# Kernel optimization log

Hardware: AMD Instinct MI355X
Metric: run time of the kernel (lower is better)

Reference implementation:

```python
import jax, jax.numpy as jnp
import numpy as np

NUM_NODES = 50000
NUM_EDGES = 800000
HIDDEN = 128
HEADS = 8
HEAD_DIM = HIDDEN // HEADS  # 16
FF_HIDDEN = 4 * HIDDEN
LN_EPS = 1e-5


def _xavier(key, shape, gain=0.01):
    fan_out, fan_in = shape
    bound = gain * np.sqrt(6.0 / (fan_in + fan_out))
    return jax.random.uniform(key, shape, jnp.float32, -bound, bound)


def setup_inputs() -> dict:
    key = jax.random.key(0)
    ks = jax.random.split(key, 10)
    x = jax.random.normal(ks[0], (NUM_NODES, HIDDEN), jnp.float32)
    edge_index = jax.random.randint(ks[1], (2, NUM_EDGES), 0, NUM_NODES, jnp.int64)
    return {
        "x": x,
        "edge_index": edge_index,
        "Wq": _xavier(ks[2], (HIDDEN, HIDDEN)),
        "bq": jnp.zeros((HIDDEN,), jnp.float32),
        "Wk": _xavier(ks[3], (HIDDEN, HIDDEN)),
        "bk": jnp.zeros((HIDDEN,), jnp.float32),
        "Wv": _xavier(ks[4], (HIDDEN, HIDDEN)),
        "bv": jnp.zeros((HIDDEN,), jnp.float32),
        "Wo": _xavier(ks[5], (HIDDEN, HIDDEN)),
        "bo": jnp.zeros((HIDDEN,), jnp.float32),
        "W1": _xavier(ks[6], (FF_HIDDEN, HIDDEN)),
        "b1": jnp.zeros((FF_HIDDEN,), jnp.float32),
        "W2": _xavier(ks[7], (HIDDEN, FF_HIDDEN)),
        "b2": jnp.zeros((HIDDEN,), jnp.float32),
        "g1": jnp.ones((HIDDEN,), jnp.float32),
        "be1": jnp.zeros((HIDDEN,), jnp.float32),
        "g2": jnp.ones((HIDDEN,), jnp.float32),
        "be2": jnp.zeros((HIDDEN,), jnp.float32),
    }


def _layernorm(v, g, b):
    mu = jnp.mean(v, axis=-1, keepdims=True)
    var = jnp.mean(jnp.square(v - mu), axis=-1, keepdims=True)
    return (v - mu) * jax.lax.rsqrt(var + LN_EPS) * g + b


def _forward(x, edge_index, Wq, bq, Wk, bk, Wv, bv, Wo, bo, W1, b1, W2, b2, g1, be1, g2, be2):
    src = edge_index[0]  # key/value side (_j)
    dst = edge_index[1]  # query side (_i), aggregation index
    scale = 1.0 / np.sqrt(HEAD_DIM)

    # Euclidean manifold: GeometricLinear == plain linear
    q = (x @ Wq.T + bq).reshape(NUM_NODES, HEADS, HEAD_DIM)
    k = (x @ Wk.T + bk).reshape(NUM_NODES, HEADS, HEAD_DIM)
    v = (x @ Wv.T + bv).reshape(NUM_NODES, HEADS, HEAD_DIM)

    # per-edge attention scores [E, H]
    alpha = jnp.einsum('ehd,ehd->eh', q[dst], k[src]) * scale
    # segment softmax over destination nodes
    m = jax.ops.segment_max(alpha, dst, num_segments=NUM_NODES)  # [N, H]
    ea = jnp.exp(alpha - m[dst])
    denom = jax.ops.segment_sum(ea, dst, num_segments=NUM_NODES)  # [N, H]
    alpha = ea / (denom[dst] + 1e-16)

    # scatter-add weighted values -> [N, H, D]
    agg = jax.ops.segment_sum(v[src] * alpha[..., None], dst, num_segments=NUM_NODES)
    att = agg.reshape(NUM_NODES, HIDDEN) @ Wo.T + bo

    # residual + norm1 (Euclidean)
    h = _layernorm(x + att, g1, be1)

    # feed-forward: fc1 -> exact GELU -> fc2
    ff = (jax.nn.gelu(h @ W1.T + b1, approximate=False)) @ W2.T + b2

    # residual + norm2
    return _layernorm(h + ff, g2, be2)


def reference(x, edge_index, Wq, bq, Wk, bk, Wv, bv, Wo, bo, W1, b1, W2, b2, g1, be1, g2, be2):
    return _forward(x, edge_index, Wq, bq, Wk, bk, Wv, bv, Wo, bo, W1, b1, W2, b2, g1, be1, g2, be2)
```

## Files before the change

### kernel.cpp

```cpp
#include <hip/hip_runtime.h>
#include <math.h>

#define N_HEADS 8
#define HEAD_DIM 16
#define HID 128
#define QKV_ROWB 512

typedef unsigned short ushort_t;
typedef __attribute__((ext_vector_type(8))) short short8;
typedef __attribute__((ext_vector_type(4))) float floatx4;
typedef __attribute__((ext_vector_type(2))) float f32x2;

#define KV_SCALE 64.0f
#define KV_INV_SCALE 0.015625f

#define W2_SCALE 65536.0f
#define A1_SCALE 512.0f
#define FF2_DESCALE (1.0f / 33554432.0f)

__device__ __forceinline__ ushort_t f2bf(float f) {
    unsigned u = __float_as_uint(f);
    unsigned r = (u + 0x7FFFu + ((u >> 16) & 1u)) >> 16;
    return (ushort_t)r;
}
__device__ __forceinline__ float bf2f(ushort_t u) {
    return __uint_as_float(((unsigned)u) << 16);
}

__device__ __forceinline__ void gld_lds16(const void* g, void* l) {
    __builtin_amdgcn_global_load_lds(
        (const __attribute__((address_space(1))) void*)g,
        (__attribute__((address_space(3))) void*)l, 16, 0, 0);
}

__device__ __forceinline__ float gelu_f(float x) {
    float z = fabsf(x) * 0.70710678118654752f;
    float t = 1.0f / (1.0f + 0.3275911f * z);
    float y = t * (0.254829592f + t * (-0.284496736f + t * (1.421413741f
            + t * (-1.453152027f + t * 1.061405429f))));
    float e = 1.0f - y * __expf(-z * z);
    e = copysignf(e, x);
    return 0.5f * x * (1.0f + e);
}

__global__ __launch_bounds__(256)
void prep_kernel(const float* __restrict__ x,
                 const float* __restrict__ Wq, const float* __restrict__ Wk,
                 const float* __restrict__ Wv, const float* __restrict__ Wo,
                 const float* __restrict__ W1, const float* __restrict__ W2,
                 const float* __restrict__ bq, const float* __restrict__ bk,
                 const float* __restrict__ bv,
                 const int* __restrict__ dst, int* __restrict__ cnt, int E,
                 ushort_t* __restrict__ xb, ushort_t* __restrict__ wts,
                 float* __restrict__ bqkv,
                 ushort_t* __restrict__ w1frag,
                 unsigned char* __restrict__ w2frag8, int xpairs)
{
    int i = blockIdx.x * 256 + threadIdx.x;
    if (i < xpairs) {
        float2 v = ((const float2*)x)[i];
        xb[i * 2]     = f2bf(v.x);
        xb[i * 2 + 1] = f2bf(v.y);
        return;
    }
    int j = i - xpairs;
    if (j < 32768) {
        const float* s; int off;
        if (j < 8192)       { s = Wq; off = j; }
        else if (j < 16384) { s = Wk; off = j - 8192; }
        else if (j < 24576) { s = Wv; off = j - 16384; }
        else                { s = Wo; off = j - 24576; }
        float2 v = ((const float2*)s)[off];
        wts[j * 2]     = f2bf(v.x);
        wts[j * 2 + 1] = f2bf(v.y);
        return;
    }
    int b = j - 32768;
    if (b < 384) {
        bqkv[b] = (b < 128) ? bq[b] : (b < 256) ? bk[b - 128] : bv[b - 256];
        return;
    }
    int c = b - 384;
    if (c < 8192) {
        int lane = c & 63, tk = c >> 6;
        int t16 = tk >> 2, kst = tk & 3;
        int row = t16 * 16 + (lane & 15);
        int kb  = kst * 32 + (lane >> 4) * 8;
        const float* s = W1 + (size_t)row * HID + kb;
        ushort_t* d = w1frag + (size_t)c * 8;
#pragma unroll
        for (int e = 0; e < 8; ++e) d[e] = f2bf(s[e]);
        return;
    }
    int c2 = c - 8192;
    if (c2 < 8192) {
        int lane = c2 & 63, tk = c2 >> 6;
        int t16 = tk >> 4, kst = tk & 15;
        int row = t16 * 16 + (lane & 15);
        int kb  = kst * 32 + (lane >> 4) * 8;
        const float* s = W2 + (size_t)row * 512 + kb;
        unsigned u0 = 0, u1 = 0;
        u0 = __builtin_amdgcn_cvt_pk_fp8_f32(s[0]*W2_SCALE, s[1]*W2_SCALE, u0, false);
        u0 = __builtin_amdgcn_cvt_pk_fp8_f32(s[2]*W2_SCALE, s[3]*W2_SCALE, u0, true);
        u1 = __builtin_amdgcn_cvt_pk_fp8_f32(s[4]*W2_SCALE, s[5]*W2_SCALE, u1, false);
        u1 = __builtin_amdgcn_cvt_pk_fp8_f32(s[6]*W2_SCALE, s[7]*W2_SCALE, u1, true);
        uint2 o; o.x = u0; o.y = u1;
        *(uint2*)(w2frag8 + (size_t)c2 * 8) = o;
        return;
    }
    int e = c2 - 8192;
    if (e < E) atomicAdd(&cnt[dst[e]], 1);
}

template<int MT, int ACT, int LN, int OUTF>
__global__ __launch_bounds__(256)
void gemm_t(const ushort_t* __restrict__ A, int lda, int M,
            const ushort_t* __restrict__ W, int K,
            const float* __restrict__ bias,
            ushort_t* __restrict__ hfragp, ushort_t* __restrict__ outb, int ostride,
            const float* __restrict__ resf, const ushort_t* __restrict__ resb,
            const float* __restrict__ g, const float* __restrict__ be)
{
    constexpr int MI   = MT / 32;
    constexpr int HALF = MT * 64 + 128 * 64;
    constexpr int BNC  = MT * 136;
    constexpr int SB   = (2 * HALF > BNC) ? 2 * HALF : BNC;
    __shared__ __align__(16) ushort_t sbuf[SB];
    __shared__ float pS[LN ? MT : 1][2];
    __shared__ float pQ[LN ? MT : 1][2];

    const int tid  = threadIdx.x;
    const int wave = tid >> 6, lane = tid & 63;
    const int gm0 = blockIdx.x * MT;
    const int o0  = blockIdx.y * 128;
    const int mhalf = wave >> 1, ohalf = wave & 1;

    auto stage = [&](int kc, int h) {
        ushort_t* As = sbuf + h * HALF;
        ushort_t* Ws = As + MT * 64;
#pragma unroll
        for (int it = 0; it < 4; ++it) {
            int s   = it * 256 + tid;
            int ln  = s & 63;
            int grp = s >> 6;
            int tile = grp >> 1, kst = grp & 1;
            int row = tile * 16 + (ln & 15);
            int kk  = kst * 32 + (ln >> 4) * 8;
            gld_lds16(&W[(size_t)(o0 + row) * K + kc + kk],
                      &Ws[(it * 256 + wave * 64) * 8]);
        }
#pragma unroll
        for (int it = 0; it < MT / 32; ++it) {
            int s   = it * 256 + tid;
            int ln  = s & 63;
            int grp = s >> 6;
            int tile = grp >> 1, kst = grp & 1;
            int row = tile * 16 + (ln & 15);
            int kk  = kst * 32 + (ln >> 4) * 8;
            int ar = gm0 + row; if (ar >= M) ar = M - 1;
            gld_lds16(&A[(size_t)ar * lda + kc + kk],
                      &As[(it * 256 + wave * 64) * 8]);
        }
    };

    floatx4 acc[MI][4];
#pragma unroll
    for (int i = 0; i < MI; ++i)
#pragma unroll
        for (int j = 0; j < 4; ++j) acc[i][j] = (floatx4)(0.f);

    const int nk = K >> 6;
    stage(0, 0);
    __syncthreads();
    for (int t = 0; t < nk; ++t) {
        if (t + 1 < nk) stage((t + 1) * 64, (t + 1) & 1);
        const ushort_t* As = sbuf + (t & 1) * HALF;
        const ushort_t* Ws = As + MT * 64;
#pragma unroll
        for (int kst = 0; kst < 2; ++kst) {
            short8 af[MI], wf[4];
#pragma unroll
            for (int i = 0; i < MI; ++i) {
                int mt = mhalf * MI + i;
                af[i] = *(const short8*)&As[((mt * 2 + kst) * 64 + lane) * 8];
            }
#pragma unroll
            for (int j = 0; j < 4; ++j) {
                int ot = ohalf * 4 + j;
                wf[j] = *(const short8*)&Ws[((ot * 2 + kst) * 64 + lane) * 8];
            }
#pragma unroll
            for (int i = 0; i < MI; ++i)
#pragma unroll
                for (int j = 0; j < 4; ++j)
                    acc[i][j] = __builtin_amdgcn_mfma_f32_16x16x32_bf16(
                        af[i], wf[j], acc[i][j], 0, 0, 0);
        }
        __syncthreads();
    }

    ushort_t* B16 = sbuf;

    if (LN) {
#pragma unroll
        for (int j = 0; j < 4; ++j) {
            int oc = (ohalf * 4 + j) * 16 + (lane & 15);
            float bj = bias[oc];
#pragma unroll
            for (int i = 0; i < MI; ++i) {
                int rbase = gm0 + (mhalf * MI + i) * 16 + (lane >> 4) * 4;
#pragma unroll
                for (int r = 0; r < 4; ++r) {
                    int rowc = rbase + r; if (rowc >= M) rowc = M - 1;
                    float rv = resb ? bf2f(resb[(size_t)rowc * HID + oc])
                                    : resf[(size_t)rowc * HID + oc];
                    acc[i][j][r] += bj + rv;
                }
            }
        }
#pragma unroll
        for (int i = 0; i < MI; ++i) {
#pragma unroll
            for (int r = 0; r < 4; ++r) {
                float s1 = acc[i][0][r] + acc[i][1][r] + acc[i][2][r] + acc[i][3][r];
                float s2 = acc[i][0][r] * acc[i][0][r] + acc[i][1][r] * acc[i][1][r]
                         + acc[i][2][r] * acc[i][2][r] + acc[i][3][r] * acc[i][3][r];
                s1 += __shfl_xor(s1, 1); s1 += __shfl_xor(s1, 2);
                s1 += __shfl_xor(s1, 4); s1 += __shfl_xor(s1, 8);
                s2 += __shfl_xor(s2, 1); s2 += __shfl_xor(s2, 2);
                s2 += __shfl_xor(s2, 4); s2 += __shfl_xor(s2, 8);
                if ((lane & 15) == 0) {
                    int rl = (mhalf * MI + i) * 16 + (lane >> 4) * 4 + r;
                    pS[rl][ohalf] = s1;
                    pQ[rl][ohalf] = s2;
                }
            }
        }
        __syncthreads();
#pragma unroll
        for (int i = 0; i < MI; ++i) {
#pragma unroll
            for (int r = 0; r < 4; ++r) {
                int rl = (mhalf * MI + i) * 16 + (lane >> 4) * 4 + r;
                float S = pS[rl][0] + pS[rl][1];
                float Q = pQ[rl][0] + pQ[rl][1];
                float mu = S * (1.f / 128.f);
                float var = Q * (1.f / 128.f) - mu * mu;
                float rstd = rsqrtf(var + 1e-5f);
#pragma unroll
                for (int j = 0; j < 4; ++j) {
                    int oc = (ohalf * 4 + j) * 16 + (lane & 15);
                    acc[i][j][r] = (acc[i][j][r] - mu) * rstd * g[oc] + be[oc];
                }
            }
        }
        __syncthreads();
    }

    if (OUTF == 0 || (OUTF == 3 && blockIdx.y == 0)) {
#pragma unroll
        for (int i = 0; i < MI; ++i)
#pragma unroll
            for (int j = 0; j < 4; ++j) {
                int oc = (ohalf * 4 + j) * 16 + (lane & 15);
                float bj = LN ? 0.f : bias[o0 + oc];
#pragma unroll
                for (int r = 0; r < 4; ++r) {
                    int rl = (mhalf * MI + i) * 16 + (lane >> 4) * 4 + r;
                    float v = acc[i][j][r] + bj;
                    if (ACT) v = gelu_f(v);
                    B16[rl * 136 + oc] = f2bf(v);
                }
            }
        __syncthreads();
        const int oo = (OUTF == 3) ? 0 : o0;
#pragma unroll
        for (int p = 0; p < MT / 16; ++p) {
            int row = p * 16 + (tid >> 4);
            int ch  = tid & 15;
            if (gm0 + row < M)
                *(short8*)&outb[(size_t)(gm0 + row) * ostride + oo + ch * 8] =
                    *(const short8*)&B16[row * 136 + ch * 8];
        }
        if (LN && hfragp) {
            int kst = tid >> 6, ln = tid & 63;
#pragma unroll
            for (int p = 0; p < MT / 16; ++p) {
                if (gm0 + p * 16 < M) {
                    int gt = (gm0 >> 4) + p;
                    short8 v = *(const short8*)&B16[(p * 16 + (ln & 15)) * 136
                                                    + kst * 32 + (ln >> 4) * 8];
                    *(short8*)&hfragp[(((size_t)gt * 4 + kst) * 64 + ln) * 8] = v;
                }
            }
        }
    } else if (OUTF == 3) {
#pragma unroll
        for (int i = 0; i < MI; ++i)
#pragma unroll
            for (int j = 0; j < 4; ++j) {
                int oc = (ohalf * 4 + j) * 16 + (lane & 15);
                float bj = bias[o0 + oc];
#pragma unroll
                for (int r = 0; r < 4; ++r) {
                    int rl = (mhalf * MI + i) * 16 + (lane >> 4) * 4 + r;
                    float v = (acc[i][j][r] + bj) * KV_SCALE;
                    B16[rl * 136 + oc] = f2bf(v);
                }
            }
        __syncthreads();
        const int koff = (blockIdx.y - 1) * 8;
#pragma unroll
        for (int p = 0; p < MT / 16; ++p) {
            int row = p * 16 + (tid >> 4);
            int ch  = tid & 15;
            if (gm0 + row < M) {
                short8 s = *(const short8*)&B16[row * 136 + ch * 8];
                unsigned u0 = 0, u1 = 0;
                u0 = __builtin_amdgcn_cvt_pk_fp8_f32(
                         bf2f((ushort_t)s[0]), bf2f((ushort_t)s[1]), u0, false);
                u0 = __builtin_amdgcn_cvt_pk_fp8_f32(
                         bf2f((ushort_t)s[2]), bf2f((ushort_t)s[3]), u0, true);
                u1 = __builtin_amdgcn_cvt_pk_fp8_f32(
                         bf2f((ushort_t)s[4]), bf2f((ushort_t)s[5]), u1, false);
                u1 = __builtin_amdgcn_cvt_pk_fp8_f32(
                         bf2f((ushort_t)s[6]), bf2f((ushort_t)s[7]), u1, true);
                uint2 o; o.x = u0; o.y = u1;
                *(uint2*)((char*)outb + (size_t)(gm0 + row) * QKV_ROWB
                          + 256 + ch * 16 + koff) = o;
            }
        }
    }
}

__global__ __launch_bounds__(256)
void ff1w_kernel(const ushort_t* __restrict__ hfrag,
                 const ushort_t* __restrict__ w1frag,
                 const float* __restrict__ b1,
                 unsigned char* __restrict__ a1img, int M)
{
    __shared__ __align__(16) ushort_t sT[4][16 * 136];
    const int wave = threadIdx.x >> 6, lane = threadIdx.x & 63;
    const int cg = wave;
    const int nt16 = (M + 15) / 16;
    const int gt0 = blockIdx.x * 2;
    const int gt1 = gt0 + 1;
    const int gt1c = (gt1 < nt16) ? gt1 : nt16 - 1;
    const int l15 = lane & 15, l4 = lane >> 4;

    floatx4 acc[2][8];
#pragma unroll
    for (int i = 0; i < 2; ++i)
#pragma unroll
        for (int j = 0; j < 8; ++j) acc[i][j] = (floatx4)(0.f);

#pragma unroll
    for (int kst = 0; kst < 4; ++kst) {
        short8 a0 = *(const short8*)&hfrag[(((size_t)gt0  * 4 + kst) * 64 + lane) * 8];
        short8 a1 = *(const short8*)&hfrag[(((size_t)gt1c * 4 + kst) * 64 + lane) * 8];
        short8 bv[8];
#pragma unroll
        for (int j = 0; j < 8; ++j)
            bv[j] = *(const short8*)&w1frag[((((size_t)cg * 8 + j) * 4 + kst) * 64 + lane) * 8];
#pragma unroll
        for (int j = 0; j < 8; ++j) {
            acc[0][j] = __builtin_amdgcn_mfma_f32_16x16x32_bf16(a0, bv[j], acc[0][j], 0, 0, 0);
            acc[1][j] = __builtin_amdgcn_mfma_f32_16x16x32_bf16(a1, bv[j], acc[1][j], 0, 0, 0);
        }
    }

    float b1v[8];
#pragma unroll
    for (int j = 0; j < 8; ++j) b1v[j] = b1[cg * 128 + j * 16 + l15];

#pragma unroll
    for (int i = 0; i < 2; ++i) {
        const int gt = i ? gt1 : gt0;
#pragma unroll
        for (int j = 0; j < 8; ++j)
#pragma unroll
            for (int r = 0; r < 4; ++r)
                sT[wave][(l4 * 4 + r) * 136 + j * 16 + l15] =
                    f2bf(gelu_f(acc[i][j][r] + b1v[j]));
        if (gt < nt16) {
#pragma unroll
            for (int q = 0; q < 4; ++q) {
                float v[8];
#pragma unroll
                for (int e = 0; e < 8; ++e)
                    v[e] = bf2f(sT[wave][l15 * 136 + q * 32 + l4 * 8 + e]) * A1_SCALE;
                unsigned u0 = 0, u1 = 0;
                u0 = __builtin_amdgcn_cvt_pk_fp8_f32(v[0], v[1], u0, false);
                u0 = __builtin_amdgcn_cvt_pk_fp8_f32(v[2], v[3], u0, true);
                u1 = __builtin_amdgcn_cvt_pk_fp8_f32(v[4], v[5], u1, false);
                u1 = __builtin_amdgcn_cvt_pk_fp8_f32(v[6], v[7], u1, true);
                uint2 o; o.x = u0; o.y = u1;
                *(uint2*)(a1img + (((size_t)gt * 16 + cg * 4 + q) * 64 + lane) * 8) = o;
            }
        }
    }
}

__global__ __launch_bounds__(256)
void ff2w_kernel(const unsigned char* __restrict__ a1img,
                 const unsigned char* __restrict__ w2frag8,
                 const ushort_t* __restrict__ hb,
                 const float* __restrict__ b2,
                 const float* __restrict__ g, const float* __restrict__ be,
                 float* __restrict__ out, int M)
{
    const int wave = threadIdx.x >> 6, lane = threadIdx.x & 63;
    const int t32 = blockIdx.x * 4 + wave;
    const int nt32 = (M + 31) / 32;
    if (t32 >= nt32) return;
    const int nt16 = (M + 15) / 16;
    const int gt0 = t32 * 2;
    const int gt1c = (gt0 + 1 < nt16) ? gt0 + 1 : nt16 - 1;
    const int l15 = lane & 15, l4 = lane >> 4;

    floatx4 acc[2][8];
#pragma unroll
    for (int i = 0; i < 2; ++i)
#pragma unroll
        for (int j = 0; j < 8; ++j) acc[i][j] = (floatx4)(0.f);

#pragma unroll
    for (int kst = 0; kst < 16; ++kst) {
        long a0 = *(const long*)(a1img + (((size_t)gt0  * 16 + kst) * 64 + lane) * 8);
        long a1 = *(const long*)(a1img + (((size_t)gt1c * 16 + kst) * 64 + lane) * 8);
        long bv[8];
#pragma unroll
        for (int j = 0; j < 8; ++j)
            bv[j] = *(const long*)(w2frag8 + (((size_t)j * 16 + kst) * 64 + lane) * 8);
#pragma unroll
        for (int j = 0; j < 8; ++j) {
            acc[0][j] = __builtin_amdgcn_mfma_f32_16x16x32_fp8_fp8(a0, bv[j], acc[0][j], 0, 0, 0);
            acc[1][j] = __builtin_amdgcn_mfma_f32_16x16x32_fp8_fp8(a1, bv[j], acc[1][j], 0, 0, 0);
        }
    }

    float b2v[8], gv[8], bev[8];
#pragma unroll
    for (int j = 0; j < 8; ++j) {
        int oc = j * 16 + l15;
        b2v[j] = b2[oc]; gv[j] = g[oc]; bev[j] = be[oc];
    }

#pragma unroll
    for (int i = 0; i < 2; ++i) {
        const int rb = (t32 * 2 + i) * 16;
#pragma unroll
        for (int j = 0; j < 8; ++j) {
            int oc = j * 16 + l15;
#pragma unroll
            for (int r = 0; r < 4; ++r) {
                int row = rb + l4 * 4 + r;
                int rc = (row < M) ? row : M - 1;
                acc[i][j][r] = acc[i][j][r] * FF2_DESCALE + b2v[j]
                             + bf2f(hb[(size_t)rc * HID + oc]);
            }
        }
#pragma unroll
        for (int r = 0; r < 4; ++r) {
            float s1 = 0.f, s2 = 0.f;
#pragma unroll
            for (int j = 0; j < 8; ++j) {
                s1 += acc[i][j][r];
                s2 += acc[i][j][r] * acc[i][j][r];
            }
            s1 += __shfl_xor(s1, 1); s1 += __shfl_xor(s1, 2);
            s1 += __shfl_xor(s1, 4); s1 += __shfl_xor(s1, 8);
            s2 += __shfl_xor(s2, 1); s2 += __shfl_xor(s2, 2);
            s2 += __shfl_xor(s2, 4); s2 += __shfl_xor(s2, 8);
            float mu = s1 * (1.f / 128.f);
            float var = s2 * (1.f / 128.f) - mu * mu;
            float rstd = rsqrtf(var + 1e-5f);
            int row = rb + l4 * 4 + r;
            if (row < M) {
#pragma unroll
                for (int j = 0; j < 8; ++j)
                    out[(size_t)row * HID + j * 16 + l15] =
                        (acc[i][j][r] - mu) * rstd * gv[j] + bev[j];
            }
        }
    }
}

__global__ __launch_bounds__(256)
void scan1_kernel(const int* __restrict__ cnt, int* __restrict__ parts, int N)
{
    __shared__ int sd[256];
    int t = threadIdx.x;
    int base = blockIdx.x * 1024 + t * 4;
    int s = 0;
#pragma unroll
    for (int j = 0; j < 4; ++j) if (base + j < N) s += cnt[base + j];
    sd[t] = s; __syncthreads();
    for (int off = 128; off; off >>= 1) {
        if (t < off) sd[t] += sd[t + off];
        __syncthreads();
    }
    if (t == 0) parts[blockIdx.x] = sd[0];
}

__global__ __launch_bounds__(256)
void scan2_kernel(const int* __restrict__ parts, int* __restrict__ poff, int nb)
{
    __shared__ int sd[256];
    int t = threadIdx.x;
    int v = (t < nb) ? parts[t] : 0;
    sd[t] = v; __syncthreads();
    for (int off = 1; off < 256; off <<= 1) {
        int u = (t >= off) ? sd[t - off] : 0;
        __syncthreads();
        sd[t] += u;
        __syncthreads();
    }
    if (t < nb) poff[t] = sd[t] - v;
}

__global__ __launch_bounds__(256)
void scan3_kernel(const int* __restrict__ cnt, const int* __restrict__ poff,
                  int* __restrict__ rp, int N)
{
    __shared__ int sd[256];
    int t = threadIdx.x;
    int base = blockIdx.x * 1024 + t * 4;
    int v0 = (base + 0 < N) ? cnt[base + 0] : 0;
    int v1 = (base + 1 < N) ? cnt[base + 1] : 0;
    int v2 = (base + 2 < N) ? cnt[base + 2] : 0;
    int v3 = (base + 3 < N) ? cnt[base + 3] : 0;
    int s = v0 + v1 + v2 + v3;
    sd[t] = s; __syncthreads();
    for (int off = 1; off < 256; off <<= 1) {
        int u = (t >= off) ? sd[t - off] : 0;
        __syncthreads();
        sd[t] += u;
        __syncthreads();
    }
    int o = poff[blockIdx.x] + sd[t] - s;
    if (base + 0 < N) rp[base + 0] = o;
    if (base + 1 < N) rp[base + 1] = o + v0;
    if (base + 2 < N) rp[base + 2] = o + v0 + v1;
    if (base + 3 < N) rp[base + 3] = o + v0 + v1 + v2;
}

__global__ __launch_bounds__(256)
void scatter_kernel(const int* __restrict__ src, const int* __restrict__ dst,
                    int* __restrict__ rp, int* __restrict__ ssrc, int E, int N)
{
    int coh = blockIdx.x & 7;
    int bc  = blockIdx.x >> 3;
    int rr  = (N + 7) >> 3;
    int nlo = coh * rr;
    int nhi = nlo + rr; if (nhi > N) nhi = N;
    int stride = (gridDim.x >> 3) * 256;
    for (int e = bc * 256 + threadIdx.x; e < E; e += stride) {
        int d = dst[e];
        if (d >= nlo && d < nhi) {
            int pos = atomicAdd(&rp[d], 1);
            ssrc[pos] = src[e];
        }
    }
}

__global__ __launch_bounds__(256)
void attn_fused_kernel(const ushort_t* __restrict__ qkvb, const int* __restrict__ rp,
                       const int* __restrict__ ssrc, ushort_t* __restrict__ aggb, int N)
{
    int wave = threadIdx.x >> 6, lane = threadIdx.x & 63;
    int n = blockIdx.x * 4 + wave;
    if (n >= N) return;
    int grp = lane >> 4;
    int cb  = (lane & 15) * 16;
    const char* base = (const char*)qkvb;

    short8 qv = *(const short8*)(base + n * QKV_ROWB + cb);
    float q[8];
#pragma unroll
    for (int j = 0; j < 8; ++j) q[j] = bf2f((ushort_t)qv[j]) * (0.25f / KV_SCALE);

    int r0 = n ? rp[n - 1] : 0;
    int r1 = rp[n];
    float acc[8] = {0.f, 0.f, 0.f, 0.f, 0.f, 0.f, 0.f, 0.f};
    float l = 0.f;

    int r = r0;
    for (; r + 8 <= r1; r += 8) {
        int s0 = ssrc[r + grp];
        int s1 = ssrc[r + 4 + grp];
        uint4 kv0 = *(const uint4*)(base + s0 * QKV_ROWB + 256 + cb);
        uint4 kv1 = *(const uint4*)(base + s1 * QKV_ROWB + 256 + cb);

        f32x2 a0 = __builtin_amdgcn_cvt_pk_f32_fp8(kv0.x, false);
        f32x2 a1 = __builtin_amdgcn_cvt_pk_f32_fp8(kv0.x, true);
        f32x2 a2 = __builtin_amdgcn_cvt_pk_f32_fp8(kv0.y, false);
        f32x2 a3 = __builtin_amdgcn_cvt_pk_f32_fp8(kv0.y, true);
        f32x2 b0 = __builtin_amdgcn_cvt_pk_f32_fp8(kv1.x, false);
        f32x2 b1 = __builtin_amdgcn_cvt_pk_f32_fp8(kv1.x, true);
        f32x2 b2 = __builtin_amdgcn_cvt_pk_f32_fp8(kv1.y, false);
        f32x2 b3 = __builtin_amdgcn_cvt_pk_f32_fp8(kv1.y, true);

        float p0 = 0.f, p1 = 0.f;
        p0 = fmaf(q[0], a0.x, p0); p0 = fmaf(q[1], a0.y, p0);
        p0 = fmaf(q[2], a1.x, p0); p0 = fmaf(q[3], a1.y, p0);
        p0 = fmaf(q[4], a2.x, p0); p0 = fmaf(q[5], a2.y, p0);
        p0 = fmaf(q[6], a3.x, p0); p0 = fmaf(q[7], a3.y, p0);
        p1 = fmaf(q[0], b0.x, p1); p1 = fmaf(q[1], b0.y, p1);
        p1 = fmaf(q[2], b1.x, p1); p1 = fmaf(q[3], b1.y, p1);
        p1 = fmaf(q[4], b2.x, p1); p1 = fmaf(q[5], b2.y, p1);
        p1 = fmaf(q[6], b3.x, p1); p1 = fmaf(q[7], b3.y, p1);

        p0 += __shfl_xor(p0, 1);
        p1 += __shfl_xor(p1, 1);
        float e0 = __expf(p0), e1 = __expf(p1);
        l += e0 + e1;

        f32x2 v0 = __builtin_amdgcn_cvt_pk_f32_fp8(kv0.z, false);
        f32x2 v1 = __builtin_amdgcn_cvt_pk_f32_fp8(kv0.z, true);
        f32x2 v2 = __builtin_amdgcn_cvt_pk_f32_fp8(kv0.w, false);
        f32x2 v3 = __builtin_amdgcn_cvt_pk_f32_fp8(kv0.w, true);
        f32x2 w0 = __builtin_amdgcn_cvt_pk_f32_fp8(kv1.z, false);
        f32x2 w1 = __builtin_amdgcn_cvt_pk_f32_fp8(kv1.z, true);
        f32x2 w2 = __builtin_amdgcn_cvt_pk_f32_fp8(kv1.w, false);
        f32x2 w3 = __builtin_amdgcn_cvt_pk_f32_fp8(kv1.w, true);

        acc[0] = fmaf(e0, v0.x, acc[0]); acc[1] = fmaf(e0, v0.y, acc[1]);
        acc[2] = fmaf(e0, v1.x, acc[2]); acc[3] = fmaf(e0, v1.y, acc[3]);
        acc[4] = fmaf(e0, v2.x, acc[4]); acc[5] = fmaf(e0, v2.y, acc[5]);
        acc[6] = fmaf(e0, v3.x, acc[6]); acc[7] = fmaf(e0, v3.y, acc[7]);
        acc[0] = fmaf(e1, w0.x, acc[0]); acc[1] = fmaf(e1, w0.y, acc[1]);
        acc[2] = fmaf(e1, w1.x, acc[2]); acc[3] = fmaf(e1, w1.y, acc[3]);
        acc[4] = fmaf(e1, w2.x, acc[4]); acc[5] = fmaf(e1, w2.y, acc[5]);
        acc[6] = fmaf(e1, w3.x, acc[6]); acc[7] = fmaf(e1, w3.y, acc[7]);
    }
    for (; r < r1; r += 4) {
        int e = r + grp;
        int s = ssrc[(e < r1) ? e : r0];
        uint4 kv = *(const uint4*)(base + s * QKV_ROWB + 256 + cb);
        f32x2 a0 = __builtin_amdgcn_cvt_pk_f32_fp8(kv.x, false);
        f32x2 a1 = __builtin_amdgcn_cvt_pk_f32_fp8(kv.x, true);
        f32x2 a2 = __builtin_amdgcn_cvt_pk_f32_fp8(kv.y, false);
        f32x2 a3 = __builtin_amdgcn_cvt_pk_f32_fp8(kv.y, true);
        float p = 0.f;
        p = fmaf(q[0], a0.x, p); p = fmaf(q[1], a0.y, p);
        p = fmaf(q[2], a1.x, p); p = fmaf(q[3], a1.y, p);
        p = fmaf(q[4], a2.x, p); p = fmaf(q[5], a2.y, p);
        p = fmaf(q[6], a3.x, p); p = fmaf(q[7], a3.y, p);
        p += __shfl_xor(p, 1);
        float ea = (e < r1) ? __expf(p) : 0.f;
        l += ea;
        f32x2 v0 = __builtin_amdgcn_cvt_pk_f32_fp8(kv.z, false);
        f32x2 v1 = __builtin_amdgcn_cvt_pk_f32_fp8(kv.z, true);
        f32x2 v2 = __builtin_amdgcn_cvt_pk_f32_fp8(kv.w, false);
        f32x2 v3 = __builtin_amdgcn_cvt_pk_f32_fp8(kv.w, true);
        acc[0] = fmaf(ea, v0.x, acc[0]); acc[1] = fmaf(ea, v0.y, acc[1]);
        acc[2] = fmaf(ea, v1.x, acc[2]); acc[3] = fmaf(ea, v1.y, acc[3]);
        acc[4] = fmaf(ea, v2.x, acc[4]); acc[5] = fmaf(ea, v2.y, acc[5]);
        acc[6] = fmaf(ea, v3.x, acc[6]); acc[7] = fmaf(ea, v3.y, acc[7]);
    }

#pragma unroll
    for (int j = 0; j < 8; ++j) {
        acc[j] += __shfl_xor(acc[j], 16);
        acc[j] += __shfl_xor(acc[j], 32);
    }
    l += __shfl_xor(l, 16);
    l += __shfl_xor(l, 32);
    float inv = KV_INV_SCALE / (l + 1e-16f);
    if (grp == 0) {
        short8 o;
#pragma unroll
        for (int j = 0; j < 8; ++j) o[j] = (short)f2bf(acc[j] * inv);
        *(short8*)((char*)aggb + n * 256 + cb) = o;
    }
}

extern "C" void kernel_launch(void* const* d_in, const int* in_sizes, int n_in,
                              void* d_out, int out_size, void* d_ws, size_t ws_size,
                              hipStream_t stream)
{
    const float* x  = (const float*)d_in[0];
    const int*   ei = (const int*)d_in[1];
    const float* Wq = (const float*)d_in[2];
    const float* bq = (const float*)d_in[3];
    const float* Wk = (const float*)d_in[4];
    const float* bk = (const float*)d_in[5];
    const float* Wv = (const float*)d_in[6];
    const float* bv = (const float*)d_in[7];
    const float* Wo = (const float*)d_in[8];
    const float* bo = (const float*)d_in[9];
    const float* W1 = (const float*)d_in[10];
    const float* b1 = (const float*)d_in[11];
    const float* W2 = (const float*)d_in[12];
    const float* b2 = (const float*)d_in[13];
    const float* g1 = (const float*)d_in[14];
    const float* be1= (const float*)d_in[15];
    const float* g2 = (const float*)d_in[16];
    const float* be2= (const float*)d_in[17];
    float* out = (float*)d_out;

    const int N = in_sizes[0] / HID;
    const int E = in_sizes[1] / 2;
    const int* srcp = ei;
    const int* dstp = ei + E;

    const size_t NH = (size_t)N * HID;
    float* wsf = (float*)d_ws;

    ushort_t* xb    = (ushort_t*)wsf;
    ushort_t* qkvb  = (ushort_t*)(wsf + NH / 2);
    ushort_t* hfrag = (ushort_t*)(wsf + NH + NH / 2);
    ushort_t* aggb  = (ushort_t*)(wsf + 2 * NH);
    ushort_t* hb    = (ushort_t*)wsf;
    unsigned char* a1img = (unsigned char*)(wsf + NH / 2);

    ushort_t* wts    = (ushort_t*)(wsf + 2 * NH + NH / 2);
    ushort_t* w1frag = wts + 65536;
    unsigned char* w2frag8 = (unsigned char*)(w1frag + 65536);
    float*    bqkv = (float*)(w2frag8 + 65536);
    int*      rp   = (int*)(bqkv + 384);
    int*      cnt  = rp + (N + 1);
    int*      poff = cnt + N;
    int*      parts= poff + 256;
    int*      ssrc = parts + 256;

    hipMemsetAsync(cnt, 0, N * sizeof(int), stream);
    const int xpairs = (int)(NH / 2);
    const int ptot   = xpairs + 32768 + 384 + 8192 + 8192 + E;
    prep_kernel<<<(ptot + 255) / 256, 256, 0, stream>>>(
        x, Wq, Wk, Wv, Wo, W1, W2, bq, bk, bv, dstp, cnt, E,
        xb, wts, bqkv, w1frag, w2frag8, xpairs);

    const int nb = (N + 1023) / 1024;
    scan1_kernel<<<nb, 256, 0, stream>>>(cnt, parts, N);
    scan2_kernel<<<1, 256, 0, stream>>>(parts, poff, nb);
    scan3_kernel<<<nb, 256, 0, stream>>>(cnt, poff, rp, N);
    scatter_kernel<<<2048, 256, 0, stream>>>(srcp, dstp, rp, ssrc, E, N);

    const int gx64 = (N + 63) / 64;
    const int nt32 = (N + 31) / 32;

    gemm_t<64, 0, 0, 3><<<dim3(gx64, 3), 256, 0, stream>>>(
        xb, HID, N, wts, HID, bqkv, nullptr, qkvb, 256,
        nullptr, nullptr, nullptr, nullptr);

    attn_fused_kernel<<<(N + 3) / 4, 256, 0, stream>>>(qkvb, rp, ssrc, aggb, N);

    gemm_t<64, 0, 1, 0><<<dim3(gx64, 1), 256, 0, stream>>>(
        aggb, HID, N, wts + 49152, HID, bo, hfrag, hb, HID,
        x, nullptr, g1, be1);

    ff1w_kernel<<<nt32, 256, 0, stream>>>(hfrag, w1frag, b1, a1img, N);

    ff2w_kernel<<<(nt32 + 3) / 4, 256, 0, stream>>>(
        a1img, w2frag8, hb, b2, g2, be2, out, N);
}
```

Before: 323.9 us.

## Replace QKV GEMM with fragment-layout wave kernel and split edge counting

Converts x and Wq/Wk/Wv into MFMA-fragment-ordered bf16 layouts in the prep kernel. A new qkvw_kernel then loads operands directly into registers without an LDS staging loop, and each wave computes two 16-row tiles against all 128 output columns. Destination-degree counting moves out of prep into a separate count_kernel whose blocks each handle only atomics landing in one eighth of the node range. The goal is to improve atomic locality and cut the generic GEMM's shared-memory traffic. The cost is re-reading dst eight times and an extra launch.

```diff
diff --git a/kernel.cpp b/kernel.cpp
--- a/kernel.cpp
+++ b/kernel.cpp
@@ -50,46 +50,61 @@
                  const float* __restrict__ W1, const float* __restrict__ W2,
                  const float* __restrict__ bq, const float* __restrict__ bk,
                  const float* __restrict__ bv,
-                 const int* __restrict__ dst, int* __restrict__ cnt, int E,
-                 ushort_t* __restrict__ xb, ushort_t* __restrict__ wts,
-                 float* __restrict__ bqkv,
+                 ushort_t* __restrict__ xfrag, ushort_t* __restrict__ woB,
+                 ushort_t* __restrict__ wqkvf,
                  ushort_t* __restrict__ w1frag,
-                 unsigned char* __restrict__ w2frag8, int xpairs)
+                 unsigned char* __restrict__ w2frag8,
+                 float* __restrict__ bqkv, int xchunks)
 {
     int i = blockIdx.x * 256 + threadIdx.x;
-    if (i < xpairs) {
-        float2 v = ((const float2*)x)[i];
-        xb[i * 2]     = f2bf(v.x);
-        xb[i * 2 + 1] = f2bf(v.y);
+    if (i < xchunks) {
+        int t16 = i >> 8;
+        int rem = i & 255;
+        int lane = rem & 63;
+        int row = t16 * 16 + (lane & 15);
+        int k   = (rem >> 6) * 32 + (lane >> 4) * 8;
+        const float* s = x + (size_t)row * HID + k;
+        short8 v;
+#pragma unroll
+        for (int e = 0; e < 8; ++e) v[e] = (short)f2bf(s[e]);
+        *(short8*)(xfrag + (size_t)i * 8) = v;
         return;
     }
-    int j = i - xpairs;
-    if (j < 32768) {
-        const float* s; int off;
-        if (j < 8192)       { s = Wq; off = j; }
-        else if (j < 16384) { s = Wk; off = j - 8192; }
-        else if (j < 24576) { s = Wv; off = j - 16384; }
-        else                { s = Wo; off = j - 24576; }
-        float2 v = ((const float2*)s)[off];
-        wts[j * 2]     = f2bf(v.x);
-        wts[j * 2 + 1] = f2bf(v.y);
+    int j = i - xchunks;
+    if (j < 8192) {
+        float2 v = ((const float2*)Wo)[j];
+        woB[j * 2]     = f2bf(v.x);
+        woB[j * 2 + 1] = f2bf(v.y);
         return;
     }
-    int b = j - 32768;
-    if (b < 384) {
-        bqkv[b] = (b < 128) ? bq[b] : (b < 256) ? bk[b - 128] : bv[b - 256];
+    int b = j - 8192;
+    if (b < 6144) {
+        int w = b >> 11;
+        int rem = b & 2047;
+        int t16 = rem >> 8;
+        int rem2 = rem & 255;
+        int lane = rem2 & 63;
+        int row = t16 * 16 + (lane & 15);
+        int k   = ((rem2 >> 6) & 3) * 32 + (lane >> 4) * 8;
+        const float* W = (w == 0) ? Wq : (w == 1) ? Wk : Wv;
+        const float* s = W + (size_t)row * HID + k;
+        short8 v;
+#pragma unroll
+        for (int e = 0; e < 8; ++e) v[e] = (short)f2bf(s[e]);
+        *(short8*)(wqkvf + (size_t)b * 8) = v;
         return;
     }
-    int c = b - 384;
+    int c = b - 6144;
     if (c < 8192) {
         int lane = c & 63, tk = c >> 6;
         int t16 = tk >> 2, kst = tk & 3;
         int row = t16 * 16 + (lane & 15);
         int kb  = kst * 32 + (lane >> 4) * 8;
         const float* s = W1 + (size_t)row * HID + kb;
-        ushort_t* d = w1frag + (size_t)c * 8;
-#pragma unroll
-        for (int e = 0; e < 8; ++e) d[e] = f2bf(s[e]);
+        short8 v;
+#pragma unroll
+        for (int e = 0; e < 8; ++e) v[e] = (short)f2bf(s[e]);
+        *(short8*)(w1frag + (size_t)c * 8) = v;
         return;
     }
     int c2 = c - 8192;
@@ -108,8 +123,108 @@
         *(uint2*)(w2frag8 + (size_t)c2 * 8) = o;
         return;
     }
-    int e = c2 - 8192;
-    if (e < E) atomicAdd(&cnt[dst[e]], 1);
+    int d = c2 - 8192;
+    if (d < 384) {
+        bqkv[d] = (d < 128) ? bq[d] : (d < 256) ? bk[d - 128] : bv[d - 256];
+    }
+}
+
+__global__ __launch_bounds__(256)
+void count_kernel(const int* __restrict__ dst, int* __restrict__ cnt, int E, int N)
+{
+    int coh = blockIdx.x & 7;
+    int bc  = blockIdx.x >> 3;
+    int rr  = (N + 7) >> 3;
+    int nlo = coh * rr;
+    int nhi = nlo + rr; if (nhi > N) nhi = N;
+    int stride = (gridDim.x >> 3) * 256;
+    for (int e = bc * 256 + threadIdx.x; e < E; e += stride) {
+        int d = dst[e];
+        if (d >= nlo && d < nhi) atomicAdd(&cnt[d], 1);
+    }
+}
+
+__global__ __launch_bounds__(256)
+void qkvw_kernel(const ushort_t* __restrict__ xfrag,
+                 const ushort_t* __restrict__ wqkvf,
+                 const float* __restrict__ bqkv,
+                 ushort_t* __restrict__ qkvb, int nt16)
+{
+    __shared__ __align__(16) ushort_t sT[4][16 * 136];
+    const int wave = threadIdx.x >> 6, lane = threadIdx.x & 63;
+    const int y = blockIdx.y;
+    const int l15 = lane & 15, l4 = lane >> 4;
+    const int gt0 = blockIdx.x * 8 + wave * 2;
+    const int gt0c = (gt0 < nt16) ? gt0 : nt16 - 1;
+    const int gt1c = (gt0 + 1 < nt16) ? gt0 + 1 : nt16 - 1;
+
+    floatx4 acc[2][8];
+#pragma unroll
+    for (int i = 0; i < 2; ++i)
+#pragma unroll
+        for (int j = 0; j < 8; ++j) acc[i][j] = (floatx4)(0.f);
+
+    const ushort_t* wf = wqkvf + (size_t)y * 16384;
+#pragma unroll
+    for (int kst = 0; kst < 4; ++kst) {
+        short8 a0 = *(const short8*)&xfrag[(((size_t)gt0c * 4 + kst) * 64 + lane) * 8];
+        short8 a1 = *(const short8*)&xfrag[(((size_t)gt1c * 4 + kst) * 64 + lane) * 8];
+        short8 bv[8];
+#pragma unroll
+        for (int j = 0; j < 8; ++j)
+            bv[j] = *(const short8*)&wf[(((size_t)j * 4 + kst) * 64 + lane) * 8];
+#pragma unroll
+        for (int j = 0; j < 8; ++j) {
+            acc[0][j] = __builtin_amdgcn_mfma_f32_16x16x32_bf16(a0, bv[j], acc[0][j], 0, 0, 0);
+            acc[1][j] = __builtin_amdgcn_mfma_f32_16x16x32_bf16(a1, bv[j], acc[1][j], 0, 0, 0);
+        }
+    }
+
+    float bb[8];
+#pragma unroll
+    for (int j = 0; j < 8; ++j) bb[j] = bqkv[y * 128 + j * 16 + l15];
+
+#pragma unroll
+    for (int i = 0; i < 2; ++i) {
+        const int gt = gt0 + i;
+#pragma unroll
+        for (int j = 0; j < 8; ++j)
+#pragma unroll
+            for (int r = 0; r < 4; ++r) {
+                float v = acc[i][j][r] + bb[j];
+                if (y) v *= KV_SCALE;
+                sT[wave][(l4 * 4 + r) * 136 + j * 16 + l15] = f2bf(v);
+            }
+        if (gt < nt16) {
+            if (y == 0) {
+#pragma unroll
+                for (int c = 0; c < 4; ++c) {
+                    int ch = l4 * 4 + c;
+                    *(short8*)&qkvb[(size_t)(gt * 16 + l15) * 256 + ch * 8] =
+                        *(const short8*)&sT[wave][l15 * 136 + ch * 8];
+                }
+            } else {
+                const int koff = (y - 1) * 8;
+#pragma unroll
+                for (int c = 0; c < 4; ++c) {
+                    int ch = l4 * 4 + c;
+                    short8 s = *(const short8*)&sT[wave][l15 * 136 + ch * 8];
+                    unsigned u0 = 0, u1 = 0;
+                    u0 = __builtin_amdgcn_cvt_pk_fp8_f32(
+                             bf2f((ushort_t)s[0]), bf2f((ushort_t)s[1]), u0, false);
+                    u0 = __builtin_amdgcn_cvt_pk_fp8_f32(
+                             bf2f((ushort_t)s[2]), bf2f((ushort_t)s[3]), u0, true);
+                    u1 = __builtin_amdgcn_cvt_pk_fp8_f32(
+                             bf2f((ushort_t)s[4]), bf2f((ushort_t)s[5]), u1, false);
+                    u1 = __builtin_amdgcn_cvt_pk_fp8_f32(
+                             bf2f((ushort_t)s[6]), bf2f((ushort_t)s[7]), u1, true);
+                    uint2 o; o.x = u0; o.y = u1;
+                    *(uint2*)((char*)qkvb + (size_t)(gt * 16 + l15) * QKV_ROWB
+                              + 256 + ch * 16 + koff) = o;
+                }
+            }
+        }
+    }
 }
 
 template<int MT, int ACT, int LN, int OUTF>
@@ -257,77 +372,38 @@
         __syncthreads();
     }
 
-    if (OUTF == 0 || (OUTF == 3 && blockIdx.y == 0)) {
-#pragma unroll
-        for (int i = 0; i < MI; ++i)
-#pragma unroll
-            for (int j = 0; j < 4; ++j) {
-                int oc = (ohalf * 4 + j) * 16 + (lane & 15);
-                float bj = LN ? 0.f : bias[o0 + oc];
-#pragma unroll
-                for (int r = 0; r < 4; ++r) {
-                    int rl = (mhalf * MI + i) * 16 + (lane >> 4) * 4 + r;
-                    float v = acc[i][j][r] + bj;
-                    if (ACT) v = gelu_f(v);
-                    B16[rl * 136 + oc] = f2bf(v);
-                }
-            }
-        __syncthreads();
-        const int oo = (OUTF == 3) ? 0 : o0;
+#pragma unroll
+    for (int i = 0; i < MI; ++i)
+#pragma unroll
+        for (int j = 0; j < 4; ++j) {
+            int oc = (ohalf * 4 + j) * 16 + (lane & 15);
+            float bj = LN ? 0.f : bias[o0 + oc];
+#pragma unroll
+            for (int r = 0; r < 4; ++r) {
+                int rl = (mhalf * MI + i) * 16 + (lane >> 4) * 4 + r;
+                float v = acc[i][j][r] + bj;
+                if (ACT) v = gelu_f(v);
+                B16[rl * 136 + oc] = f2bf(v);
+            }
+        }
+    __syncthreads();
+#pragma unroll
+    for (int p = 0; p < MT / 16; ++p) {
+        int row = p * 16 + (tid >> 4);
+        int ch  = tid & 15;
+        if (gm0 + row < M)
+            *(short8*)&outb[(size_t)(gm0 + row) * ostride + o0 + ch * 8] =
+                *(const short8*)&B16[row * 136 + ch * 8];
+    }
+    if (LN && hfragp) {
+        int kst = tid >> 6, ln = tid & 63;
 #pragma unroll
         for (int p = 0; p < MT / 16; ++p) {
-            int row = p * 16 + (tid >> 4);
-            int ch  = tid & 15;
-            if (gm0 + row < M)
-                *(short8*)&outb[(size_t)(gm0 + row) * ostride + oo + ch * 8] =
-                    *(const short8*)&B16[row * 136 + ch * 8];
-        }
-        if (LN && hfragp) {
-            int kst = tid >> 6, ln = tid & 63;
-#pragma unroll
-            for (int p = 0; p < MT / 16; ++p) {
-                if (gm0 + p * 16 < M) {
-                    int gt = (gm0 >> 4) + p;
-                    short8 v = *(const short8*)&B16[(p * 16 + (ln & 15)) * 136
-                                                    + kst * 32 + (ln >> 4) * 8];
-                    *(short8*)&hfragp[(((size_t)gt * 4 + kst) * 64 + ln) * 8] = v;
-                }
-            }
-        }
-    } else if (OUTF == 3) {
-#pragma unroll
-        for (int i = 0; i < MI; ++i)
-#pragma unroll
-            for (int j = 0; j < 4; ++j) {
-                int oc = (ohalf * 4 + j) * 16 + (lane & 15);
-                float bj = bias[o0 + oc];
-#pragma unroll
-                for (int r = 0; r < 4; ++r) {
-                    int rl = (mhalf * MI + i) * 16 + (lane >> 4) * 4 + r;
-                    float v = (acc[i][j][r] + bj) * KV_SCALE;
-                    B16[rl * 136 + oc] = f2bf(v);
-                }
-            }
-        __syncthreads();
-        const int koff = (blockIdx.y - 1) * 8;
-#pragma unroll
-        for (int p = 0; p < MT / 16; ++p) {
-            int row = p * 16 + (tid >> 4);
-            int ch  = tid & 15;
-            if (gm0 + row < M) {
-                short8 s = *(const short8*)&B16[row * 136 + ch * 8];
-                unsigned u0 = 0, u1 = 0;
-                u0 = __builtin_amdgcn_cvt_pk_fp8_f32(
-                         bf2f((ushort_t)s[0]), bf2f((ushort_t)s[1]), u0, false);
-                u0 = __builtin_amdgcn_cvt_pk_fp8_f32(
-                         bf2f((ushort_t)s[2]), bf2f((ushort_t)s[3]), u0, true);
-                u1 = __builtin_amdgcn_cvt_pk_fp8_f32(
-                         bf2f((ushort_t)s[4]), bf2f((ushort_t)s[5]), u1, false);
-                u1 = __builtin_amdgcn_cvt_pk_fp8_f32(
-                         bf2f((ushort_t)s[6]), bf2f((ushort_t)s[7]), u1, true);
-                uint2 o; o.x = u0; o.y = u1;
-                *(uint2*)((char*)outb + (size_t)(gm0 + row) * QKV_ROWB
-                          + 256 + ch * 16 + koff) = o;
+            if (gm0 + p * 16 < M) {
+                int gt = (gm0 >> 4) + p;
+                short8 v = *(const short8*)&B16[(p * 16 + (ln & 15)) * 136
+                                                + kst * 32 + (ln >> 4) * 8];
+                *(short8*)&hfragp[(((size_t)gt * 4 + kst) * 64 + ln) * 8] = v;
             }
         }
     }
@@ -708,16 +784,21 @@
     const size_t NH = (size_t)N * HID;
     float* wsf = (float*)d_ws;
 
-    ushort_t* xb    = (ushort_t*)wsf;
+    const int nt16 = (N + 15) / 16;
+    const int nt32 = (N + 31) / 32;
+
+    ushort_t* xfrag = (ushort_t*)wsf;
     ushort_t* qkvb  = (ushort_t*)(wsf + NH / 2);
     ushort_t* hfrag = (ushort_t*)(wsf + NH + NH / 2);
     ushort_t* aggb  = (ushort_t*)(wsf + 2 * NH);
     ushort_t* hb    = (ushort_t*)wsf;
     unsigned char* a1img = (unsigned char*)(wsf + NH / 2);
 
-    ushort_t* wts    = (ushort_t*)(wsf + 2 * NH + NH / 2);
-    ushort_t* w1frag = wts + 65536;
-    unsigned char* w2frag8 = (unsigned char*)(w1frag + 65536);
+    ushort_t* U       = (ushort_t*)(wsf + 2 * NH + NH / 2);
+    ushort_t* woB     = U;
+    ushort_t* wqkvf   = U + 16384;
+    ushort_t* w1frag  = U + 65536;
+    unsigned char* w2frag8 = (unsigned char*)(U + 131072);
     float*    bqkv = (float*)(w2frag8 + 65536);
     int*      rp   = (int*)(bqkv + 384);
     int*      cnt  = rp + (N + 1);
@@ -726,29 +807,27 @@
     int*      ssrc = parts + 256;
 
     hipMemsetAsync(cnt, 0, N * sizeof(int), stream);
-    const int xpairs = (int)(NH / 2);
-    const int ptot   = xpairs + 32768 + 384 + 8192 + 8192 + E;
+    const int xchunks = nt16 * 256;
+    const int ptot = xchunks + 8192 + 6144 + 8192 + 8192 + 384;
     prep_kernel<<<(ptot + 255) / 256, 256, 0, stream>>>(
-        x, Wq, Wk, Wv, Wo, W1, W2, bq, bk, bv, dstp, cnt, E,
-        xb, wts, bqkv, w1frag, w2frag8, xpairs);
-
+        x, Wq, Wk, Wv, Wo, W1, W2, bq, bk, bv,
+        xfrag, woB, wqkvf, w1frag, w2frag8, bqkv, xchunks);
+
+    count_kernel<<<2048, 256, 0, stream>>>(dstp, cnt, E, N);
     const int nb = (N + 1023) / 1024;
     scan1_kernel<<<nb, 256, 0, stream>>>(cnt, parts, N);
     scan2_kernel<<<1, 256, 0, stream>>>(parts, poff, nb);
     scan3_kernel<<<nb, 256, 0, stream>>>(cnt, poff, rp, N);
     scatter_kernel<<<2048, 256, 0, stream>>>(srcp, dstp, rp, ssrc, E, N);
 
+    qkvw_kernel<<<dim3((nt16 + 7) / 8, 3), 256, 0, stream>>>(
+        xfrag, wqkvf, bqkv, qkvb, nt16);
+
+    attn_fused_kernel<<<(N + 3) / 4, 256, 0, stream>>>(qkvb, rp, ssrc, aggb, N);
+
     const int gx64 = (N + 63) / 64;
-    const int nt32 = (N + 31) / 32;
-
-    gemm_t<64, 0, 0, 3><<<dim3(gx64, 3), 256, 0, stream>>>(
-        xb, HID, N, wts, HID, bqkv, nullptr, qkvb, 256,
-        nullptr, nullptr, nullptr, nullptr);
-
-    attn_fused_kernel<<<(N + 3) / 4, 256, 0, stream>>>(qkvb, rp, ssrc, aggb, N);
-
     gemm_t<64, 0, 1, 0><<<dim3(gx64, 1), 256, 0, stream>>>(
-        aggb, HID, N, wts + 49152, HID, bo, hfrag, hb, HID,
+        aggb, HID, N, woB, HID, bo, hfrag, hb, HID,
         x, nullptr, g1, be1);
 
     ff1w_kernel<<<nt32, 256, 0, stream>>>(hfrag, w1frag, b1, a1img, N);
```

Result: no change. 322.4 us (-0.5%).
